# Optimization experiments

Measured on AMD Instinct MI355X. Metric: run time of the kernel, lower is better.

The kernel has to match this reference:

```python
import math
import jax, jax.numpy as jnp
import numpy as np

N_LAYER = 4
D = 192        # n_embd
NH = 4         # n_head
N = 3072       # n_neurons = n_embd * mlp_dim_mult // n_head
VOCAB = 256
BLOCK = 4096
EPS = 1e-5
B, T = 1, 1024


def get_freqs(n, theta=2.0 ** 16):
    t = np.arange(n, dtype=np.float32)
    q = np.floor(t / 2.0) * 2.0  # quantize(t, 2)
    return (1.0 / theta ** (q / n) / (2.0 * math.pi)).astype(np.float32)

_FREQS = jnp.asarray(get_freqs(N))  # [N]


def _ln(x):
    # LayerNorm over last dim, no affine (elementwise_affine=False)
    m = jnp.mean(x, axis=-1, keepdims=True)
    v = jnp.var(x, axis=-1, keepdims=True)
    return (x - m) / jnp.sqrt(v + EPS)


def _rope(x):
    # x: [B, nh, T, N]
    t = x.shape[2]
    phases = (jnp.arange(t, dtype=jnp.float32)[:, None] * _FREQS[None, :]) % 1.0 * (2.0 * math.pi)  # [T, N]
    x_even = x[..., 0::2]
    x_odd = x[..., 1::2]
    v_rot = jnp.stack((-x_odd, x_even), axis=-1).reshape(x.shape)
    return x * jnp.cos(phases) + v_rot * jnp.sin(phases)


def setup_inputs() -> dict:
    key = jax.random.key(0)
    ks = jax.random.split(key, 7)
    s = 0.02
    return {
        "idx": jax.random.randint(ks[0], (B, T), 0, VOCAB, dtype=jnp.int64)
        if jax.config.jax_enable_x64 else jax.random.randint(ks[0], (B, T), 0, VOCAB, dtype=jnp.int32),
        "decoder_x": jax.random.normal(ks[1], (NH, D, N), jnp.float32) * s,
        "decoder_y": jax.random.normal(ks[2], (NH, D, N), jnp.float32) * s,
        "encoder": jax.random.normal(ks[3], (NH * N, D), jnp.float32) * s,
        "embed": jax.random.normal(ks[4], (VOCAB, D), jnp.float32) * s,
        "pos_emb": jax.random.normal(ks[5], (BLOCK, D), jnp.float32) * s,
        "lm_head": jax.random.normal(ks[6], (D, VOCAB), jnp.float32) * s,
    }


def reference(idx, decoder_x, decoder_y, encoder, embed, pos_emb, lm_head):
    b, t = idx.shape
    x = embed[idx] + pos_emb[:t][None]          # [B, T, D]
    x = _ln(x)
    mask = jnp.tril(jnp.ones((t, t), jnp.float32), k=-1)  # strictly lower
    for _ in range(N_LAYER):
        # encoder-side sparsification: D -> N per head
        x_sparse = jax.nn.relu(jnp.einsum('btd,hdn->bhtn', x, decoder_x))  # [B,nh,T,N]
        qr = _rope(x_sparse)
        scores = jnp.einsum('bhtn,bhsn->bhts', qr, qr) * mask              # [B,nh,T,T]
        ykv = _ln(jnp.einsum('bhts,bsd->bhtd', scores, x))                 # [B,nh,T,D]
        y_sparse = jax.nn.relu(jnp.einsum('bhtd,hdn->bhtn', ykv, decoder_y))
        xy = x_sparse * y_sparse                                           # [B,nh,T,N]
        # [B,T,nh*N] @ [nh*N, D]
        ymlp = jnp.einsum('bhtn,hnd->btd', xy, encoder.reshape(NH, N, D))
        x = _ln(x + _ln(ymlp))
    logits = jnp.einsum('btd,dv->btv', x, lm_head)                         # [B,T,vocab]
    return logits
```

## Files before the change

### kernel.cpp

```cpp
#include <hip/hip_runtime.h>
#include <hip/hip_bf16.h>

using bf16 = __hip_bfloat16;

#define D_DIM   192
#define N_DIM   3072
#define NHEAD   4
#define T_SEQ   1024
#define HN      12288
#define NP2     1536
#define VOCABSZ 256
#define NLAYER  4
#define LN_EPS  1e-5f
#define TWO_PI  6.2831853071795864f

typedef __attribute__((ext_vector_type(8)))  short          s16x8;
typedef __attribute__((ext_vector_type(8)))  unsigned short u16x8;
typedef __attribute__((ext_vector_type(4)))  float          f32x4;
typedef __attribute__((ext_vector_type(16))) float          f32x16;

__device__ __forceinline__ float b2f(bf16 v) { return __bfloat162float(v); }
__device__ __forceinline__ float us2f(unsigned short u) {
    unsigned int x = ((unsigned int)u) << 16;
    return __builtin_bit_cast(float, x);
}
__device__ __forceinline__ unsigned short f2us(float f) {
    bf16 b = __float2bfloat16(f);
    return __builtin_bit_cast(unsigned short, b);
}

__global__ void fill_out(float* __restrict__ out, float val, int nelem) {
    int i = blockIdx.x * 256 + threadIdx.x;
    if (i < nelem) out[i] = val;
}

__global__ void t_cvt(const float* __restrict__ in, bf16* __restrict__ out,
                      int R, int C, long inZ, long outZ) {
    __shared__ float tile[64][65];
    in  += inZ  * blockIdx.z;
    out += outZ * blockIdx.z;
    const int tx = threadIdx.x & 63, ty = threadIdx.x >> 6;
    const int r0 = blockIdx.y * 64, c0 = blockIdx.x * 64;
    #pragma unroll
    for (int rr = 0; rr < 16; rr++) {
        int row = ty * 16 + rr;
        tile[row][tx] = in[(size_t)(r0 + row) * C + c0 + tx];
    }
    __syncthreads();
    #pragma unroll
    for (int rr = 0; rr < 16; rr++) {
        int row = ty * 16 + rr;
        out[(size_t)(c0 + row) * R + r0 + tx] = __float2bfloat16(tile[tx][row]);
    }
}

__device__ __forceinline__ void wave_sum2(float& s, float& ss) {
    #pragma unroll
    for (int off = 1; off < 64; off <<= 1) {
        s  += __shfl_xor(s,  off, 64);
        ss += __shfl_xor(ss, off, 64);
    }
}

__global__ void k_embed(const int* __restrict__ idx, const float* __restrict__ emb,
                        const float* __restrict__ pos, float* __restrict__ x,
                        bf16* __restrict__ xb) {
    int t = blockIdx.x, l = threadIdx.x;
    int tok = idx[t];
    const float* e = emb + tok * D_DIM;
    const float* p = pos + t * D_DIM;
    float v0 = e[l] + p[l], v1 = e[l + 64] + p[l + 64], v2 = e[l + 128] + p[l + 128];
    float s = v0 + v1 + v2, ss = v0 * v0 + v1 * v1 + v2 * v2;
    wave_sum2(s, ss);
    float m = s / D_DIM, r = rsqrtf(ss / D_DIM - m * m + LN_EPS);
    float* xr = x + t * D_DIM;
    bf16*  xo = xb + (size_t)t * D_DIM;
    float o0 = (v0 - m) * r, o1 = (v1 - m) * r, o2 = (v2 - m) * r;
    xr[l] = o0; xr[l + 64] = o1; xr[l + 128] = o2;
    xo[l] = __float2bfloat16(o0);
    xo[l + 64] = __float2bfloat16(o1);
    xo[l + 128] = __float2bfloat16(o2);
}

__global__ void k_ln(float* __restrict__ buf) {
    int l = threadIdx.x;
    float* row = buf + (size_t)blockIdx.x * D_DIM;
    float v0 = row[l], v1 = row[l + 64], v2 = row[l + 128];
    float s = v0 + v1 + v2, ss = v0 * v0 + v1 * v1 + v2 * v2;
    wave_sum2(s, ss);
    float m = s / D_DIM, r = rsqrtf(ss / D_DIM - m * m + LN_EPS);
    row[l] = (v0 - m) * r; row[l + 64] = (v1 - m) * r; row[l + 128] = (v2 - m) * r;
}

__global__ void k_ln2b(const float* __restrict__ P0, const float* __restrict__ P1,
                       bf16* __restrict__ outb) {
    int l = threadIdx.x;
    size_t off = (size_t)blockIdx.x * D_DIM;
    const float* r0 = P0 + off;
    const float* r1 = P1 + off;
    float v0 = r0[l] + r1[l];
    float v1 = r0[l + 64] + r1[l + 64];
    float v2 = r0[l + 128] + r1[l + 128];
    float s = v0 + v1 + v2, ss = v0 * v0 + v1 * v1 + v2 * v2;
    wave_sum2(s, ss);
    float m = s / D_DIM, r = rsqrtf(ss / D_DIM - m * m + LN_EPS);
    bf16* o = outb + off;
    o[l]       = __float2bfloat16((v0 - m) * r);
    o[l + 64]  = __float2bfloat16((v1 - m) * r);
    o[l + 128] = __float2bfloat16((v2 - m) * r);
}

template <int NSLAB>
__global__ void k_resid(float* __restrict__ x, const float* __restrict__ P,
                        bf16* __restrict__ xb) {
    int l = threadIdx.x, t = blockIdx.x;
    float y0 = 0.f, y1 = 0.f, y2 = 0.f;
    #pragma unroll
    for (int p = 0; p < NSLAB; p++) {
        const float* r = P + (size_t)p * T_SEQ * D_DIM + (size_t)t * D_DIM;
        y0 += r[l]; y1 += r[l + 64]; y2 += r[l + 128];
    }
    float* xr = x + (size_t)t * D_DIM;
    float s = y0 + y1 + y2, ss = y0 * y0 + y1 * y1 + y2 * y2;
    wave_sum2(s, ss);
    float m1 = s / D_DIM, r1 = rsqrtf(ss / D_DIM - m1 * m1 + LN_EPS);
    float v0 = xr[l] + (y0 - m1) * r1;
    float v1 = xr[l + 64] + (y1 - m1) * r1;
    float v2 = xr[l + 128] + (y2 - m1) * r1;
    s = v0 + v1 + v2; ss = v0 * v0 + v1 * v1 + v2 * v2;
    wave_sum2(s, ss);
    float m2 = s / D_DIM, r2 = rsqrtf(ss / D_DIM - m2 * m2 + LN_EPS);
    float o0 = (v0 - m2) * r2, o1 = (v1 - m2) * r2, o2 = (v2 - m2) * r2;
    xr[l] = o0; xr[l + 64] = o1; xr[l + 128] = o2;
    bf16* xo = xb + (size_t)t * D_DIM;
    xo[l] = __float2bfloat16(o0);
    xo[l + 64] = __float2bfloat16(o1);
    xo[l + 128] = __float2bfloat16(o2);
}

__global__ void k_tables(ushort2* __restrict__ csT) {
    int gid = blockIdx.x * 256 + threadIdx.x;
    int t = gid / NP2, p = gid % NP2;
    float qf = (float)(2 * p);
    float f = exp2f(qf * (-16.0f / 3072.0f)) * (1.0f / (float)TWO_PI);
    float ph = fmodf((float)t * f, 1.0f) * (float)TWO_PI;
    ushort2 cs;
    cs.x = f2us(cosf(ph));
    cs.y = f2us(sinf(ph));
    csT[gid] = cs;
}

__launch_bounds__(256, 4)
__global__ void scores64(const bf16* __restrict__ qr, bf16* __restrict__ sc,
                         bf16* __restrict__ dbuf) {
    const int bid = blockIdx.x;
    const int xcd = bid & 7;
    const int h   = xcd >> 1;
    const int kh  = xcd & 1;
    const int L   = bid >> 3;
    int i = 0;
    while (((i + 1) * (i + 2)) >> 1 <= L) ++i;
    int j = L - ((i * (i + 1)) >> 1);
    const int t0 = i * 64, s0 = j * 64;
    const bool diag = (i == j);

    int arow = t0, brow = s0;
    if (kh == 1 && !diag) { arow = s0; brow = t0; }

    __shared__ short As[2][64][72];
    __shared__ short Bs[2][64][72];

    const int tid = threadIdx.x;
    const int lane = tid & 63, w = tid >> 6;
    const int wtm = (w >> 1) * 32, wtn = (w & 1) * 32;
    const int l31 = lane & 31, lhi = lane >> 5;
    const int r0 = tid >> 2;
    const int kq = (tid & 3) * 16;

    const int kBeg = kh * (N_DIM / 2);
    const bf16* gA = qr + (size_t)(arow + r0) * HN + h * N_DIM + kBeg + kq;
    const bf16* gB = qr + (size_t)(brow + r0) * HN + h * N_DIM + kBeg + kq;

    u16x8 pa0, pa1, pb0, pb1;
    u16x8 qa0, qa1, qb0, qb1;
    auto load0 = [&](int k0) {
        pa0 = *(const u16x8*)(gA + k0);
        pa1 = *(const u16x8*)(gA + k0 + 8);
        pb0 = *(const u16x8*)(gB + k0);
        pb1 = *(const u16x8*)(gB + k0 + 8);
    };
    auto load1 = [&](int k0) {
        qa0 = *(const u16x8*)(gA + k0);
        qa1 = *(const u16x8*)(gA + k0 + 8);
        qb0 = *(const u16x8*)(gB + k0);
        qb1 = *(const u16x8*)(gB + k0 + 8);
    };
    auto dep0 = [&](int buf) {
        *(u16x8*)&As[buf][r0][kq]     = pa0;
        *(u16x8*)&As[buf][r0][kq + 8] = pa1;
        *(u16x8*)&Bs[buf][r0][kq]     = pb0;
        *(u16x8*)&Bs[buf][r0][kq + 8] = pb1;
    };
    auto dep1 = [&](int buf) {
        *(u16x8*)&As[buf][r0][kq]     = qa0;
        *(u16x8*)&As[buf][r0][kq + 8] = qa1;
        *(u16x8*)&Bs[buf][r0][kq]     = qb0;
        *(u16x8*)&Bs[buf][r0][kq + 8] = qb1;
    };

    f32x16 acc;
    #pragma unroll
    for (int r = 0; r < 16; r++) acc[r] = 0.f;

    auto mfma_step = [&](int buf) {
        #pragma unroll
        for (int ks = 0; ks < 4; ks++) {
            s16x8 a = *(const s16x8*)&As[buf][wtm + l31][ks * 16 + lhi * 8];
            s16x8 b = *(const s16x8*)&Bs[buf][wtn + l31][ks * 16 + lhi * 8];
            acc = __builtin_amdgcn_mfma_f32_32x32x16_bf16(a, b, acc, 0, 0, 0);
        }
    };

    const int NIT = (N_DIM / 2) / 64;
    load0(0);
    load1(64);
    dep0(0);
    __syncthreads();

    for (int k = 0; k < NIT; k += 2) {
        if (k + 2 < NIT) load0((k + 2) * 64);
        mfma_step(0);
        if (k + 1 < NIT) dep1(1);
        __syncthreads();
        if (k + 1 < NIT) {
            if (k + 3 < NIT) load1((k + 3) * 64);
            mfma_step(1);
            if (k + 2 < NIT) dep0(0);
            __syncthreads();
        }
    }

    __syncthreads();
    short (*S)[72] = (short(*)[72])&As[0][0][0];
    const bool trS = (kh == 1) && !diag;
    #pragma unroll
    for (int r = 0; r < 16; r++) {
        int rr = wtm + (r & 3) + 8 * (r >> 2) + 4 * lhi;
        int cc = wtn + l31;
        float v = acc[r];
        if (diag && cc >= rr) v = 0.f;
        if (trS) S[cc][rr] = (short)f2us(v);
        else     S[rr][cc] = (short)f2us(v);
    }
    __syncthreads();
    if (kh == 1 && diag) {
        bf16* P = dbuf + (size_t)(h * 16 + i) * 4096;
        #pragma unroll
        for (int e = 0; e < 2; e++) {
            int idxe = tid + e * 256;
            int row = idxe >> 3, cg = (idxe & 7) * 8;
            u16x8 v = *(const u16x8*)&S[row][cg];
            *(u16x8*)(P + row * 64 + cg) = v;
        }
    } else {
        bf16* C = sc + (size_t)h * T_SEQ * T_SEQ;
        #pragma unroll
        for (int e = 0; e < 2; e++) {
            int idxe = tid + e * 256;
            int row = idxe >> 3, cg = (idxe & 7) * 8;
            u16x8 v = *(const u16x8*)&S[row][cg];
            *(u16x8*)(C + (size_t)(arow + row) * T_SEQ + brow + cg) = v;
        }
    }
}

__device__ __forceinline__ void stage_rope8(short* dst, const bf16* src,
                                            const ushort2* csP) {
    u16x8 v  = *(const u16x8*)src;
    u16x8 cs = *(const u16x8*)csP;
    u16x8 o;
    #pragma unroll
    for (int i = 0; i < 4; i++) {
        float e  = us2f(v[2 * i]), od = us2f(v[2 * i + 1]);
        float c  = us2f(cs[2 * i]), s = us2f(cs[2 * i + 1]);
        o[2 * i]     = f2us(e * c - od * s);
        o[2 * i + 1] = f2us(od * c + e * s);
    }
    *(u16x8*)dst = o;
}

__launch_bounds__(256)
__global__ void scores_fused(const bf16* __restrict__ xs,
                             const ushort2* __restrict__ csT,
                             bf16* __restrict__ sc) {
    const int h  = blockIdx.z;
    const int s0 = blockIdx.x * 64, t0 = blockIdx.y * 64;
    if (s0 > t0) return;
    __shared__ short As[64][40];
    __shared__ short Bs[64][40];
    const int tid  = threadIdx.x;
    const int srow = tid >> 2, kq = (tid & 3) * 8;
    const int lane = tid & 63, w = tid >> 6, qd = lane >> 4, lc = lane & 15;
    const int tA = t0 + srow, tB = s0 + srow;
    const bf16* gA = xs + (size_t)tA * HN + h * N_DIM + kq;
    const bf16* gB = xs + (size_t)tB * HN + h * N_DIM + kq;
    const ushort2* cA = csT + (size_t)tA * NP2 + (kq >> 1);
    const ushort2* cB = csT + (size_t)tB * NP2 + (kq >> 1);
    f32x4 acc[4] = {{0.f,0.f,0.f,0.f},{0.f,0.f,0.f,0.f},
                    {0.f,0.f,0.f,0.f},{0.f,0.f,0.f,0.f}};
    for (int k0 = 0; k0 < N_DIM; k0 += 32) {
        stage_rope8(&As[srow][kq], gA + k0, cA + (k0 >> 1));
        stage_rope8(&Bs[srow][kq], gB + k0, cB + (k0 >> 1));
        __syncthreads();
        s16x8 a = *(const s16x8*)&As[w * 16 + lc][qd * 8];
        #pragma unroll
        for (int j = 0; j < 4; j++) {
            s16x8 b = *(const s16x8*)&Bs[j * 16 + lc][qd * 8];
            acc[j] = __builtin_amdgcn_mfma_f32_16x16x32_bf16(a, b, acc[j], 0, 0, 0);
        }
        __syncthreads();
    }
    bf16* C = sc + (size_t)h * T_SEQ * T_SEQ;
    const bool diag = (s0 == t0);
    const int tbase = t0 + w * 16 + qd * 4;
    #pragma unroll
    for (int j = 0; j < 4; j++) {
        int s = s0 + j * 16 + lc;
        #pragma unroll
        for (int r = 0; r < 4; r++) {
            int t = tbase + r;
            C[(size_t)t * T_SEQ + s] =
                __float2bfloat16((!diag || s < t) ? acc[j][r] : 0.f);
        }
    }
}

template <int EPI, bool WQR, typename TA>
__launch_bounds__(256)
__global__ void dgemm128(const TA* __restrict__ A, const bf16* __restrict__ Bt,
                         bf16* __restrict__ xs, bf16* __restrict__ qr,
                         const ushort2* __restrict__ csT) {
    __shared__ __align__(16) short pool[2 * 2 * 128 * 40];
    short (*As)[128][40] = (short(*)[128][40])pool;
    short (*Bs)[128][40] = (short(*)[128][40])(pool + 2 * 128 * 40);

    const int tid = threadIdx.x;
    const int lane = tid & 63, w = tid >> 6;
    const int l31 = lane & 31, lhi = lane >> 5;
    const int wtm = (w >> 1) * 64, wtn = (w & 1) * 64;
    const int n0 = blockIdx.x * 128, m0 = blockIdx.y * 128;
    if constexpr (EPI == 2) A += (size_t)(n0 / N_DIM) * T_SEQ * D_DIM;

    const int r0 = tid >> 2, r1 = r0 + 64;
    const int kq = (tid & 3) * 8;

    const TA*   gA = A  + kq;
    const bf16* gB = Bt + kq;

    float4 fa00, fa01, fa02, fa03, fa10, fa11, fa12, fa13;
    u16x8 ba00, ba01, ba10, ba11;
    u16x8 pb00, pb01, pb10, pb11;
    auto load0 = [&](int k0) {
        if constexpr (__is_same(TA, float)) {
            const TA* a0 = gA + (size_t)(m0 + r0) * D_DIM + k0;
            const TA* a1 = gA + (size_t)(m0 + r1) * D_DIM + k0;
            fa00 = *(const float4*)a0; fa01 = *(const float4*)(a0 + 4);
            fa02 = *(const float4*)a1; fa03 = *(const float4*)(a1 + 4);
        } else {
            ba00 = *(const u16x8*)(gA + (size_t)(m0 + r0) * D_DIM + k0);
            ba01 = *(const u16x8*)(gA + (size_t)(m0 + r1) * D_DIM + k0);
        }
        pb00 = *(const u16x8*)(gB + (size_t)(n0 + r0) * D_DIM + k0);
        pb01 = *(const u16x8*)(gB + (size_t)(n0 + r1) * D_DIM + k0);
    };
    auto load1 = [&](int k0) {
        if constexpr (__is_same(TA, float)) {
            const TA* a0 = gA + (size_t)(m0 + r0) * D_DIM + k0;
            const TA* a1 = gA + (size_t)(m0 + r1) * D_DIM + k0;
            fa10 = *(const float4*)a0; fa11 = *(const float4*)(a0 + 4);
            fa12 = *(const float4*)a1; fa13 = *(const float4*)(a1 + 4);
        } else {
            ba10 = *(const u16x8*)(gA + (size_t)(m0 + r0) * D_DIM + k0);
            ba11 = *(const u16x8*)(gA + (size_t)(m0 + r1) * D_DIM + k0);
        }
        pb10 = *(const u16x8*)(gB + (size_t)(n0 + r0) * D_DIM + k0);
        pb11 = *(const u16x8*)(gB + (size_t)(n0 + r1) * D_DIM + k0);
    };
    auto dep0 = [&](int buf) {
        if constexpr (__is_same(TA, float)) {
            u16x8 o0, o1;
            o0[0] = f2us(fa00.x); o0[1] = f2us(fa00.y); o0[2] = f2us(fa00.z); o0[3] = f2us(fa00.w);
            o0[4] = f2us(fa01.x); o0[5] = f2us(fa01.y); o0[6] = f2us(fa01.z); o0[7] = f2us(fa01.w);
            o1[0] = f2us(fa02.x); o1[1] = f2us(fa02.y); o1[2] = f2us(fa02.z); o1[3] = f2us(fa02.w);
            o1[4] = f2us(fa03.x); o1[5] = f2us(fa03.y); o1[6] = f2us(fa03.z); o1[7] = f2us(fa03.w);
            *(u16x8*)&As[buf][r0][kq] = o0;
            *(u16x8*)&As[buf][r1][kq] = o1;
        } else {
            *(u16x8*)&As[buf][r0][kq] = ba00;
            *(u16x8*)&As[buf][r1][kq] = ba01;
        }
        *(u16x8*)&Bs[buf][r0][kq] = pb00;
        *(u16x8*)&Bs[buf][r1][kq] = pb01;
    };
    auto dep1 = [&](int buf) {
        if constexpr (__is_same(TA, float)) {
            u16x8 o0, o1;
            o0[0] = f2us(fa10.x); o0[1] = f2us(fa10.y); o0[2] = f2us(fa10.z); o0[3] = f2us(fa10.w);
            o0[4] = f2us(fa11.x); o0[5] = f2us(fa11.y); o0[6] = f2us(fa11.z); o0[7] = f2us(fa11.w);
            o1[0] = f2us(fa12.x); o1[1] = f2us(fa12.y); o1[2] = f2us(fa12.z); o1[3] = f2us(fa12.w);
            o1[4] = f2us(fa13.x); o1[5] = f2us(fa13.y); o1[6] = f2us(fa13.z); o1[7] = f2us(fa13.w);
            *(u16x8*)&As[buf][r0][kq] = o0;
            *(u16x8*)&As[buf][r1][kq] = o1;
        } else {
            *(u16x8*)&As[buf][r0][kq] = ba10;
            *(u16x8*)&As[buf][r1][kq] = ba11;
        }
        *(u16x8*)&Bs[buf][r0][kq] = pb10;
        *(u16x8*)&Bs[buf][r1][kq] = pb11;
    };

    f32x16 acc00, acc01, acc10, acc11;
    #pragma unroll
    for (int r = 0; r < 16; r++) { acc00[r] = 0.f; acc01[r] = 0.f; acc10[r] = 0.f; acc11[r] = 0.f; }

    auto mfma_step = [&](int buf) {
        #pragma unroll
        for (int ks = 0; ks < 2; ks++) {
            s16x8 a0 = *(const s16x8*)&As[buf][wtm + l31][ks * 16 + lhi * 8];
            s16x8 a1 = *(const s16x8*)&As[buf][wtm + 32 + l31][ks * 16 + lhi * 8];
            s16x8 b0 = *(const s16x8*)&Bs[buf][wtn + l31][ks * 16 + lhi * 8];
            s16x8 b1 = *(const s16x8*)&Bs[buf][wtn + 32 + l31][ks * 16 + lhi * 8];
            acc00 = __builtin_amdgcn_mfma_f32_32x32x16_bf16(a0, b0, acc00, 0, 0, 0);
            acc01 = __builtin_amdgcn_mfma_f32_32x32x16_bf16(a0, b1, acc01, 0, 0, 0);
            acc10 = __builtin_amdgcn_mfma_f32_32x32x16_bf16(a1, b0, acc10, 0, 0, 0);
            acc11 = __builtin_amdgcn_mfma_f32_32x32x16_bf16(a1, b1, acc11, 0, 0, 0);
        }
    };

    const int NIT = D_DIM / 32;
    load0(0);
    load1(32);
    dep0(0);
    __syncthreads();
    for (int k = 0; k < NIT; k += 2) {
        if (k + 2 < NIT) load0((k + 2) * 32);
        mfma_step(0);
        if (k + 1 < NIT) dep1(1);
        __syncthreads();
        if (k + 1 < NIT) {
            if (k + 3 < NIT) load1((k + 3) * 32);
            mfma_step(1);
            if (k + 2 < NIT) dep0(0);
            __syncthreads();
        }
    }

    short (*S)[136] = (short(*)[136])pool;
    #pragma unroll
    for (int r = 0; r < 16; r++) {
        int rb = (r & 3) + 8 * (r >> 2) + 4 * lhi;
        S[wtm + rb     ][wtn + l31     ] = (short)f2us(fmaxf(acc00[r], 0.f));
        S[wtm + rb     ][wtn + 32 + l31] = (short)f2us(fmaxf(acc01[r], 0.f));
        S[wtm + 32 + rb][wtn + l31     ] = (short)f2us(fmaxf(acc10[r], 0.f));
        S[wtm + 32 + rb][wtn + 32 + l31] = (short)f2us(fmaxf(acc11[r], 0.f));
    }
    __syncthreads();
    #pragma unroll
    for (int e = 0; e < 8; e++) {
        int idxe = tid + e * 256;
        int row = idxe >> 4, cg = idxe & 15;
        u16x8 v = *(const u16x8*)&S[row][cg * 8];
        int t = m0 + row, ngg = n0 + cg * 8;
        size_t ci = (size_t)t * HN + ngg;
        if constexpr (EPI == 1) {
            *(u16x8*)(xs + ci) = v;
            if constexpr (WQR) {
                int p0 = (ngg % N_DIM) >> 1;
                u16x8 cs8 = *(const u16x8*)&csT[(size_t)t * NP2 + p0];
                u16x8 o;
                #pragma unroll
                for (int q = 0; q < 4; q++) {
                    float ev = us2f(v[2 * q]), ov = us2f(v[2 * q + 1]);
                    float c = us2f(cs8[2 * q]), s = us2f(cs8[2 * q + 1]);
                    o[2 * q]     = f2us(ev * c - ov * s);
                    o[2 * q + 1] = f2us(ov * c + ev * s);
                }
                *(u16x8*)(qr + ci) = o;
            }
        } else {
            u16x8 g = *(const u16x8*)(xs + ci);
            u16x8 o;
            #pragma unroll
            for (int q = 0; q < 8; q++) o[q] = f2us(us2f(g[q]) * us2f(v[q]));
            *(u16x8*)(xs + ci) = o;
        }
    }
}

__launch_bounds__(256, 2)
__global__ void gate_ymlp(const bf16* __restrict__ ykvb, const bf16* __restrict__ wY,
                          const bf16* __restrict__ xs, const bf16* __restrict__ wE,
                          float* __restrict__ P) {
    const int bid = blockIdx.x;
    const int s   = (bid & 7) + ((bid >> 7) << 3);
    const int tb  = (bid >> 3) & 15;
    const int t0  = tb * 64;
    const int h   = s >> 2;
    const int ng0 = s * 768;
    const int nh0 = (s & 3) * 768;

    __shared__ __align__(16) short A1s[64][200];
    __shared__ __align__(16) short Bsh[192][72];
    __shared__ __align__(16) short xyA[64][72];
    short (*B1)[200] = (short(*)[200])&Bsh[0][0];

    const int tid = threadIdx.x;
    const int lane = tid & 63, w = tid >> 6;
    const int l31 = lane & 31, lhi = lane >> 5;
    const int wm  = (w >> 1) * 32;
    const int wn1 = (w & 1) * 32;
    const int wn2 = (w & 1) * 96;

    {
        const bf16* src = ykvb + ((size_t)h * T_SEQ + t0 + (tid >> 2)) * D_DIM
                        + (tid & 3) * 48;
        #pragma unroll
        for (int j = 0; j < 6; j++) {
            u16x8 v = *(const u16x8*)(src + j * 8);
            *(u16x8*)&A1s[tid >> 2][(tid & 3) * 48 + j * 8] = v;
        }
    }

    f32x16 oc0, oc1, oc2;
    #pragma unroll
    for (int r = 0; r < 16; r++) { oc0[r] = 0.f; oc1[r] = 0.f; oc2[r] = 0.f; }

    __syncthreads();

    for (int c = 0; c < 12; c++) {
        const int nc = c * 64;
        {
            const bf16* src = wY + ((size_t)h * N_DIM + nh0 + nc + (tid >> 2)) * D_DIM
                            + (tid & 3) * 48;
            #pragma unroll
            for (int j = 0; j < 6; j++) {
                u16x8 v = *(const u16x8*)(src + j * 8);
                *(u16x8*)&B1[tid >> 2][(tid & 3) * 48 + j * 8] = v;
            }
        }
        __syncthreads();
        f32x16 ys;
        #pragma unroll
        for (int r = 0; r < 16; r++) ys[r] = 0.f;
        #pragma unroll
        for (int ks = 0; ks < 12; ks++) {
            s16x8 a = *(const s16x8*)&A1s[wm + l31][ks * 16 + lhi * 8];
            s16x8 b = *(const s16x8*)&B1[wn1 + l31][ks * 16 + lhi * 8];
            ys = __builtin_amdgcn_mfma_f32_32x32x16_bf16(a, b, ys, 0, 0, 0);
        }
        __syncthreads();
        #pragma unroll
        for (int r = 0; r < 16; r++) {
            int rr = wm + (r & 3) + 8 * (r >> 2) + 4 * lhi;
            xyA[rr][wn1 + l31] = (short)f2us(fmaxf(ys[r], 0.f));
        }
        __syncthreads();
        {
            int row = tid >> 2, c0l = (tid & 3) * 16;
            const bf16* sx = xs + (size_t)(t0 + row) * HN + ng0 + nc + c0l;
            #pragma unroll
            for (int e = 0; e < 2; e++) {
                u16x8 g = *(const u16x8*)(sx + e * 8);
                u16x8 y = *(const u16x8*)&xyA[row][c0l + e * 8];
                u16x8 o;
                #pragma unroll
                for (int q = 0; q < 8; q++) o[q] = f2us(us2f(g[q]) * us2f(y[q]));
                *(u16x8*)&xyA[row][c0l + e * 8] = o;
            }
        }
        {
            #pragma unroll
            for (int j = 0; j < 3; j++) {
                int d  = (tid >> 2) * 3 + j;
                int cc = (tid & 3) * 16;
                const bf16* src = wE + (size_t)d * HN + ng0 + nc + cc;
                u16x8 v0 = *(const u16x8*)src;
                u16x8 v1 = *(const u16x8*)(src + 8);
                *(u16x8*)&Bsh[d][cc]     = v0;
                *(u16x8*)&Bsh[d][cc + 8] = v1;
            }
        }
        __syncthreads();
        #pragma unroll
        for (int ks = 0; ks < 4; ks++) {
            s16x8 a  = *(const s16x8*)&xyA[wm + l31][ks * 16 + lhi * 8];
            s16x8 b0 = *(const s16x8*)&Bsh[wn2 + l31     ][ks * 16 + lhi * 8];
            s16x8 b1 = *(const s16x8*)&Bsh[wn2 + 32 + l31][ks * 16 + lhi * 8];
            s16x8 b2 = *(const s16x8*)&Bsh[wn2 + 64 + l31][ks * 16 + lhi * 8];
            oc0 = __builtin_amdgcn_mfma_f32_32x32x16_bf16(a, b0, oc0, 0, 0, 0);
            oc1 = __builtin_amdgcn_mfma_f32_32x32x16_bf16(a, b1, oc1, 0, 0, 0);
            oc2 = __builtin_amdgcn_mfma_f32_32x32x16_bf16(a, b2, oc2, 0, 0, 0);
        }
        __syncthreads();
    }

    float* O = P + (size_t)s * T_SEQ * D_DIM;
    #pragma unroll
    for (int r = 0; r < 16; r++) {
        int rt = t0 + wm + (r & 3) + 8 * (r >> 2) + 4 * lhi;
        O[(size_t)rt * D_DIM + wn2 +      l31] = oc0[r];
        O[(size_t)rt * D_DIM + wn2 + 32 + l31] = oc1[r];
        O[(size_t)rt * D_DIM + wn2 + 64 + l31] = oc2[r];
    }
}

template <typename TA, int MODE>
__launch_bounds__(256)
__global__ void mfma_gemm(const TA* __restrict__ A, const bf16* __restrict__ Bt,
                          float* __restrict__ C, const bf16* __restrict__ aux,
                          int K, int kSeg, int lda, int ldb, int ldc,
                          long aZ, long bZ, long cZ) {
    constexpr bool DUAL = (MODE == 1);
    constexpr int TILES = DUAL ? 6 : 4;
    __shared__ __align__(16) short pool[TILES * 64 * 72];
    short (*As)[64][72] = (short(*)[64][72])pool;
    short (*Bs)[64][72] = (short(*)[64][72])(pool + 2 * 64 * 72);
    short (*Ms)[64][72] = (short(*)[64][72])(pool + 4 * 64 * 72);

    int bx, by, z;
    if constexpr (MODE == 1) {
        const int bid  = blockIdx.x;
        z = bid & 7;
        const int rest = bid >> 3;
        bx = rest % 3;
        by = rest / 3;
    } else {
        bx = blockIdx.x; by = blockIdx.y; z = blockIdx.z;
    }

    const int tid = threadIdx.x;
    const int n0 = bx * 64, m0 = by * 64;
    const int srow = tid >> 2, sk = (tid & 3) * 16;
    const int lane = tid & 63, w = tid >> 6;
    const int l31 = lane & 31, lhi = lane >> 5;
    const int wm = (w >> 1) * 32, wn = (w & 1) * 32;

    int kBeg, kEnd, zh = 0;
    if constexpr (MODE == 1) {
        zh = z >> 1;
        const int seg = z & 1;
        A += aZ * zh;
        C += cZ * zh + bZ * seg;
        const int kc = (m0 + 64 < K) ? m0 + 64 : K;
        const int half0 = ((kc + 127) >> 7) << 6;
        kBeg = seg ? half0 : 0;
        kEnd = seg ? kc : half0;
    } else if constexpr (MODE == 2) {
        A += aZ * z; Bt += bZ * z; C += cZ * z;
        kBeg = z * kSeg; kEnd = kBeg + kSeg;
    } else if constexpr (MODE == 3) {
        A += aZ * z; Bt += bZ * z; C += cZ * z;
        kBeg = 0; kEnd = (m0 + 64 < K) ? m0 + 64 : K;
    } else {
        A += aZ * z; Bt += bZ * z; C += cZ * z;
        kBeg = 0; kEnd = K;
    }

    const TA*   ga = A  + (size_t)(m0 + srow) * lda + sk;
    const bf16* gb = Bt + (size_t)(n0 + srow) * ldb + sk;

    auto msrc = [&](int k0) -> const bf16* {
        if (k0 == m0)
            return aux + (size_t)(zh * 16 + (m0 >> 6)) * 4096
                       + (size_t)srow * 64 + sk;
        return (const bf16*)A + (size_t)(k0 + srow) * lda + m0 + sk;
    };

    float4 f00, f01, f02, f03, f10, f11, f12, f13;
    u16x8 pa00, pa01, pa10, pa11, pb00, pb01, pb10, pb11;
    u16x8 pm00, pm01, pm10, pm11;
    auto load0 = [&](int k0) {
        if constexpr (__is_same(TA, float)) {
            f00 = *(const float4*)(ga + k0);
            f01 = *(const float4*)(ga + k0 + 4);
            f02 = *(const float4*)(ga + k0 + 8);
            f03 = *(const float4*)(ga + k0 + 12);
        } else {
            pa00 = *(const u16x8*)(ga + k0);
            pa01 = *(const u16x8*)(ga + k0 + 8);
        }
        pb00 = *(const u16x8*)(gb + k0);
        pb01 = *(const u16x8*)(gb + k0 + 8);
        if constexpr (DUAL) {
            const bf16* ms = msrc(k0);
            pm00 = *(const u16x8*)ms;
            pm01 = *(const u16x8*)(ms + 8);
        }
    };
    auto load1 = [&](int k0) {
        if constexpr (__is_same(TA, float)) {
            f10 = *(const float4*)(ga + k0);
            f11 = *(const float4*)(ga + k0 + 4);
            f12 = *(const float4*)(ga + k0 + 8);
            f13 = *(const float4*)(ga + k0 + 12);
        } else {
            pa10 = *(const u16x8*)(ga + k0);
            pa11 = *(const u16x8*)(ga + k0 + 8);
        }
        pb10 = *(const u16x8*)(gb + k0);
        pb11 = *(const u16x8*)(gb + k0 + 8);
        if constexpr (DUAL) {
            const bf16* ms = msrc(k0);
            pm10 = *(const u16x8*)ms;
            pm11 = *(const u16x8*)(ms + 8);
        }
    };
    auto dep0 = [&](int buf) {
        if constexpr (__is_same(TA, float)) {
            u16x8 o0, o1;
            o0[0] = f2us(f00.x); o0[1] = f2us(f00.y); o0[2] = f2us(f00.z); o0[3] = f2us(f00.w);
            o0[4] = f2us(f01.x); o0[5] = f2us(f01.y); o0[6] = f2us(f01.z); o0[7] = f2us(f01.w);
            o1[0] = f2us(f02.x); o1[1] = f2us(f02.y); o1[2] = f2us(f02.z); o1[3] = f2us(f02.w);
            o1[4] = f2us(f03.x); o1[5] = f2us(f03.y); o1[6] = f2us(f03.z); o1[7] = f2us(f03.w);
            *(u16x8*)&As[buf][srow][sk]     = o0;
            *(u16x8*)&As[buf][srow][sk + 8] = o1;
        } else {
            *(u16x8*)&As[buf][srow][sk]     = pa00;
            *(u16x8*)&As[buf][srow][sk + 8] = pa01;
        }
        *(u16x8*)&Bs[buf][srow][sk]     = pb00;
        *(u16x8*)&Bs[buf][srow][sk + 8] = pb01;
        if constexpr (DUAL) {
            *(u16x8*)&Ms[buf][srow][sk]     = pm00;
            *(u16x8*)&Ms[buf][srow][sk + 8] = pm01;
        }
    };
    auto dep1 = [&](int buf) {
        if constexpr (__is_same(TA, float)) {
            u16x8 o0, o1;
            o0[0] = f2us(f10.x); o0[1] = f2us(f10.y); o0[2] = f2us(f10.z); o0[3] = f2us(f10.w);
            o0[4] = f2us(f11.x); o0[5] = f2us(f11.y); o0[6] = f2us(f11.z); o0[7] = f2us(f11.w);
            o1[0] = f2us(f12.x); o1[1] = f2us(f12.y); o1[2] = f2us(f12.z); o1[3] = f2us(f12.w);
            o1[4] = f2us(f13.x); o1[5] = f2us(f13.y); o1[6] = f2us(f13.z); o1[7] = f2us(f13.w);
            *(u16x8*)&As[buf][srow][sk]     = o0;
            *(u16x8*)&As[buf][srow][sk + 8] = o1;
        } else {
            *(u16x8*)&As[buf][srow][sk]     = pa10;
            *(u16x8*)&As[buf][srow][sk + 8] = pa11;
        }
        *(u16x8*)&Bs[buf][srow][sk]     = pb10;
        *(u16x8*)&Bs[buf][srow][sk + 8] = pb11;
        if constexpr (DUAL) {
            *(u16x8*)&Ms[buf][srow][sk]     = pm10;
            *(u16x8*)&Ms[buf][srow][sk + 8] = pm11;
        }
    };

    f32x16 acc;
    #pragma unroll
    for (int r = 0; r < 16; r++) acc[r] = 0.f;

    auto mfma_step = [&](int buf) {
        #pragma unroll
        for (int ks = 0; ks < 4; ks++) {
            s16x8 a = *(const s16x8*)&As[buf][wm + l31][ks * 16 + lhi * 8];
            s16x8 b = *(const s16x8*)&Bs[buf][wn + l31][ks * 16 + lhi * 8];
            acc = __builtin_amdgcn_mfma_f32_32x32x16_bf16(a, b, acc, 0, 0, 0);
            if constexpr (DUAL) {
                s16x8 m2 = *(const s16x8*)&Ms[buf][wm + l31][ks * 16 + lhi * 8];
                acc = __builtin_amdgcn_mfma_f32_32x32x16_bf16(m2, b, acc, 0, 0, 0);
            }
        }
    };

    const int NIT = (kEnd - kBeg) >> 6;
    load0(kBeg);
    load1(kBeg + 64);
    dep0(0);
    __syncthreads();

    for (int k = 0; k < NIT; k += 2) {
        if (k + 2 < NIT) load0(kBeg + (k + 2) * 64);
        mfma_step(0);
        if (k + 1 < NIT) dep1(1);
        __syncthreads();
        if (k + 1 < NIT) {
            if (k + 3 < NIT) load1(kBeg + (k + 3) * 64);
            mfma_step(1);
            if (k + 2 < NIT) dep0(0);
            __syncthreads();
        }
    }

    #pragma unroll
    for (int r = 0; r < 16; r++) {
        int row = m0 + wm + (r & 3) + 8 * (r >> 2) + 4 * lhi;
        int col = n0 + wn + l31;
        C[(size_t)row * ldc + col] = acc[r];
    }
}

extern "C" void kernel_launch(void* const* d_in, const int* in_sizes, int n_in,
                              void* d_out, int out_size, void* d_ws, size_t ws_size,
                              hipStream_t stream) {
    const int*   idx   = (const int*)  d_in[0];
    const float* dec_x = (const float*)d_in[1];
    const float* dec_y = (const float*)d_in[2];
    const float* enc   = (const float*)d_in[3];
    const float* emb   = (const float*)d_in[4];
    const float* pose  = (const float*)d_in[5];
    const float* lmh   = (const float*)d_in[6];
    float* out = (float*)d_out;

    char* wp = (char*)d_ws;
    float*   x    = (float*)wp;              wp += (size_t)T_SEQ * D_DIM * 4;
    bf16*    xs   = (bf16*)wp;               wp += (size_t)T_SEQ * HN * 2;
    ushort2* csT  = (ushort2*)wp;            wp += (size_t)T_SEQ * NP2 * 4;
    bf16*    sc   = (bf16*)wp;               wp += (size_t)NHEAD * T_SEQ * T_SEQ * 2;
    float*   ykv  = (float*)wp;              wp += (size_t)NHEAD * T_SEQ * D_DIM * 4;
    float*   ymlp = (float*)wp;              wp += (size_t)T_SEQ * D_DIM * 4;
    bf16*    xT   = (bf16*)wp;               wp += (size_t)D_DIM * T_SEQ * 2;
    bf16*    wX   = (bf16*)wp;               wp += (size_t)NHEAD * N_DIM * D_DIM * 2;
    bf16*    wY   = (bf16*)wp;               wp += (size_t)NHEAD * N_DIM * D_DIM * 2;
    bf16*    wE   = (bf16*)wp;               wp += (size_t)D_DIM * HN * 2;
    bf16*    wL   = (bf16*)wp;               wp += (size_t)VOCABSZ * D_DIM * 2;
    const size_t BASE_NEED = (size_t)(wp - (char*)d_ws);
    bf16*    qr   = (bf16*)wp;
    const size_t FULL_NEED = BASE_NEED + (size_t)T_SEQ * HN * 2;
    bf16*  dbuf  = (bf16*)ymlp;

    if (ws_size < BASE_NEED) {
        fill_out<<<(out_size + 255) / 256, 256, 0, stream>>>(out, (float)ws_size, out_size);
        return;
    }
    const bool USE_QR = (ws_size >= FULL_NEED);

    bf16*  xb_main = (bf16*)sc;
    bf16*  xb_fb   = (bf16*)ymlp;
    float* ymlpP16 = (float*)qr;
    bf16*  ykvb    = (bf16*)((char*)qr + (size_t)16 * T_SEQ * D_DIM * 4);
    float* ymlpP8  = (float*)sc;

    bf16* xb = USE_QR ? xb_main : xb_fb;

    t_cvt<<<dim3(48, 3, 4), 256, 0, stream>>>(dec_x, wX, D_DIM, N_DIM,
                                              (long)D_DIM * N_DIM, (long)N_DIM * D_DIM);
    t_cvt<<<dim3(48, 3, 4), 256, 0, stream>>>(dec_y, wY, D_DIM, N_DIM,
                                              (long)D_DIM * N_DIM, (long)N_DIM * D_DIM);
    t_cvt<<<dim3(3, 192, 1), 256, 0, stream>>>(enc, wE, HN, D_DIM, 0L, 0L);
    t_cvt<<<dim3(4, 3, 1), 256, 0, stream>>>(lmh, wL, D_DIM, VOCABSZ, 0L, 0L);

    k_tables<<<(T_SEQ * NP2) / 256, 256, 0, stream>>>(csT);
    k_embed<<<T_SEQ, 64, 0, stream>>>(idx, emb, pose, x, xb);

    for (int l = 0; l < NLAYER; ++l) {
        t_cvt<<<dim3(3, 16, 1), 256, 0, stream>>>(x, xT, T_SEQ, D_DIM, 0L, 0L);
        if (USE_QR) {
            dgemm128<1, true, bf16><<<dim3(96, 8), 256, 0, stream>>>(xb, wX, xs, qr, csT);
            scores64<<<dim3(1088), 256, 0, stream>>>(qr, sc, dbuf);
            long segZ = (long)((float*)qr - ykv);
            mfma_gemm<bf16, 1><<<dim3(384), 256, 0, stream>>>(
                sc, xT, ykv, dbuf, T_SEQ, 0, T_SEQ, T_SEQ, D_DIM,
                (long)T_SEQ * T_SEQ, segZ, (long)T_SEQ * D_DIM);
            k_ln2b<<<NHEAD * T_SEQ, 64, 0, stream>>>(ykv, (const float*)qr, ykvb);
            gate_ymlp<<<dim3(256), 256, 0, stream>>>(ykvb, wY, xs, wE, ymlpP16);
            k_resid<16><<<T_SEQ, 64, 0, stream>>>(x, ymlpP16, xb);
        } else {
            dgemm128<1, false, bf16><<<dim3(96, 8), 256, 0, stream>>>(xb, wX, xs, qr, csT);
            scores_fused<<<dim3(16, 16, NHEAD), 256, 0, stream>>>(xs, csT, sc);
            mfma_gemm<bf16, 3><<<dim3(3, 16, NHEAD), 256, 0, stream>>>(
                sc, xT, ykv, nullptr, T_SEQ, 0, T_SEQ, T_SEQ, D_DIM,
                (long)T_SEQ * T_SEQ, 0L, (long)T_SEQ * D_DIM);
            k_ln<<<NHEAD * T_SEQ, 64, 0, stream>>>(ykv);
            dgemm128<2, false, float><<<dim3(96, 8), 256, 0, stream>>>(
                ykv, wY, xs, nullptr, nullptr);
            mfma_gemm<bf16, 2><<<dim3(3, 16, 8), 256, 0, stream>>>(
                xs, wE, ymlpP8, nullptr, HN, HN / 8, HN, HN, D_DIM,
                0L, 0L, (long)T_SEQ * D_DIM);
            k_resid<8><<<T_SEQ, 64, 0, stream>>>(x, ymlpP8, xb);
        }
    }

    mfma_gemm<float, 0><<<dim3(4, 16, 1), 256, 0, stream>>>(
        x, wL, out, nullptr, D_DIM, 0, D_DIM, D_DIM, VOCABSZ, 0L, 0L, 0L);
}
```

Measured before the change: 467.9 us.

## Fuse xT transpose into residual LN and fold ykv LayerNorm into gate kernel

Removes the per-layer x transpose kernel by having the embedding and residual LayerNorm kernels write the bf16 transposed copy directly. Also removes the separate k_ln2b kernel by summing the two split-K ykv partials and applying LayerNorm inside gate_ymlp's A-tile load. This cuts kernel launches and an intermediate bf16 buffer round trip. In exchange it adds strided, uncoalesced 2-byte column stores, redundant LN work across blocks sharing the same rows, and more registers in gate_ymlp.

New measurement: 466.4 us. Within noise of the previous version (-0.3%).

```diff
diff --git a/kernel.cpp b/kernel.cpp
--- a/kernel.cpp
+++ b/kernel.cpp
@@ -64,7 +64,7 @@
 
 __global__ void k_embed(const int* __restrict__ idx, const float* __restrict__ emb,
                         const float* __restrict__ pos, float* __restrict__ x,
-                        bf16* __restrict__ xb) {
+                        bf16* __restrict__ xb, bf16* __restrict__ xT) {
     int t = blockIdx.x, l = threadIdx.x;
     int tok = idx[t];
     const float* e = emb + tok * D_DIM;
@@ -77,9 +77,12 @@
     bf16*  xo = xb + (size_t)t * D_DIM;
     float o0 = (v0 - m) * r, o1 = (v1 - m) * r, o2 = (v2 - m) * r;
     xr[l] = o0; xr[l + 64] = o1; xr[l + 128] = o2;
-    xo[l] = __float2bfloat16(o0);
-    xo[l + 64] = __float2bfloat16(o1);
-    xo[l + 128] = __float2bfloat16(o2);
+    bf16 b0 = __float2bfloat16(o0), b1 = __float2bfloat16(o1), b2 = __float2bfloat16(o2);
+    xo[l] = b0; xo[l + 64] = b1; xo[l + 128] = b2;
+    bf16* col = xT + t;
+    col[(size_t)l * T_SEQ]         = b0;
+    col[(size_t)(l + 64) * T_SEQ]  = b1;
+    col[(size_t)(l + 128) * T_SEQ] = b2;
 }
 
 __global__ void k_ln(float* __restrict__ buf) {
@@ -92,27 +95,9 @@
     row[l] = (v0 - m) * r; row[l + 64] = (v1 - m) * r; row[l + 128] = (v2 - m) * r;
 }
 
-__global__ void k_ln2b(const float* __restrict__ P0, const float* __restrict__ P1,
-                       bf16* __restrict__ outb) {
-    int l = threadIdx.x;
-    size_t off = (size_t)blockIdx.x * D_DIM;
-    const float* r0 = P0 + off;
-    const float* r1 = P1 + off;
-    float v0 = r0[l] + r1[l];
-    float v1 = r0[l + 64] + r1[l + 64];
-    float v2 = r0[l + 128] + r1[l + 128];
-    float s = v0 + v1 + v2, ss = v0 * v0 + v1 * v1 + v2 * v2;
-    wave_sum2(s, ss);
-    float m = s / D_DIM, r = rsqrtf(ss / D_DIM - m * m + LN_EPS);
-    bf16* o = outb + off;
-    o[l]       = __float2bfloat16((v0 - m) * r);
-    o[l + 64]  = __float2bfloat16((v1 - m) * r);
-    o[l + 128] = __float2bfloat16((v2 - m) * r);
-}
-
 template <int NSLAB>
 __global__ void k_resid(float* __restrict__ x, const float* __restrict__ P,
-                        bf16* __restrict__ xb) {
+                        bf16* __restrict__ xb, bf16* __restrict__ xT) {
     int l = threadIdx.x, t = blockIdx.x;
     float y0 = 0.f, y1 = 0.f, y2 = 0.f;
     #pragma unroll
@@ -132,10 +117,13 @@
     float m2 = s / D_DIM, r2 = rsqrtf(ss / D_DIM - m2 * m2 + LN_EPS);
     float o0 = (v0 - m2) * r2, o1 = (v1 - m2) * r2, o2 = (v2 - m2) * r2;
     xr[l] = o0; xr[l + 64] = o1; xr[l + 128] = o2;
+    bf16 b0 = __float2bfloat16(o0), b1 = __float2bfloat16(o1), b2 = __float2bfloat16(o2);
     bf16* xo = xb + (size_t)t * D_DIM;
-    xo[l] = __float2bfloat16(o0);
-    xo[l + 64] = __float2bfloat16(o1);
-    xo[l + 128] = __float2bfloat16(o2);
+    xo[l] = b0; xo[l + 64] = b1; xo[l + 128] = b2;
+    bf16* col = xT + t;
+    col[(size_t)l * T_SEQ]         = b0;
+    col[(size_t)(l + 64) * T_SEQ]  = b1;
+    col[(size_t)(l + 128) * T_SEQ] = b2;
 }
 
 __global__ void k_tables(ushort2* __restrict__ csT) {
@@ -498,7 +486,8 @@
 }
 
 __launch_bounds__(256, 2)
-__global__ void gate_ymlp(const bf16* __restrict__ ykvb, const bf16* __restrict__ wY,
+__global__ void gate_ymlp(const float* __restrict__ ykv0, const float* __restrict__ ykv1,
+                          const bf16* __restrict__ wY,
                           const bf16* __restrict__ xs, const bf16* __restrict__ wE,
                           float* __restrict__ P) {
     const int bid = blockIdx.x;
@@ -522,12 +511,30 @@
     const int wn2 = (w & 1) * 96;
 
     {
-        const bf16* src = ykvb + ((size_t)h * T_SEQ + t0 + (tid >> 2)) * D_DIM
-                        + (tid & 3) * 48;
-        #pragma unroll
-        for (int j = 0; j < 6; j++) {
-            u16x8 v = *(const u16x8*)(src + j * 8);
-            *(u16x8*)&A1s[tid >> 2][(tid & 3) * 48 + j * 8] = v;
+        const int row = tid >> 2, q = tid & 3;
+        size_t off = ((size_t)h * T_SEQ + t0 + row) * D_DIM + q * 48;
+        const float* p0 = ykv0 + off;
+        const float* p1 = ykv1 + off;
+        float v[48];
+        float sm = 0.f, ssq = 0.f;
+        #pragma unroll
+        for (int e = 0; e < 12; e++) {
+            float4 a = *(const float4*)(p0 + e * 4);
+            float4 b = *(const float4*)(p1 + e * 4);
+            float c0 = a.x + b.x, c1 = a.y + b.y, c2 = a.z + b.z, c3 = a.w + b.w;
+            v[e * 4 + 0] = c0; v[e * 4 + 1] = c1; v[e * 4 + 2] = c2; v[e * 4 + 3] = c3;
+            sm  += c0 + c1 + c2 + c3;
+            ssq += c0 * c0 + c1 * c1 + c2 * c2 + c3 * c3;
+        }
+        sm  += __shfl_xor(sm, 1, 64);  ssq += __shfl_xor(ssq, 1, 64);
+        sm  += __shfl_xor(sm, 2, 64);  ssq += __shfl_xor(ssq, 2, 64);
+        float m = sm / D_DIM, r = rsqrtf(ssq / D_DIM - m * m + LN_EPS);
+        #pragma unroll
+        for (int e = 0; e < 6; e++) {
+            u16x8 o;
+            #pragma unroll
+            for (int k2 = 0; k2 < 8; k2++) o[k2] = f2us((v[e * 8 + k2] - m) * r);
+            *(u16x8*)&A1s[row][q * 48 + e * 8] = o;
         }
     }
 
@@ -838,7 +845,7 @@
     bf16*  xb_main = (bf16*)sc;
     bf16*  xb_fb   = (bf16*)ymlp;
     float* ymlpP16 = (float*)qr;
-    bf16*  ykvb    = (bf16*)((char*)qr + (size_t)16 * T_SEQ * D_DIM * 4);
+    float* ykvP1   = (float*)((char*)qr + (size_t)16 * T_SEQ * D_DIM * 4);
     float* ymlpP8  = (float*)sc;
 
     bf16* xb = USE_QR ? xb_main : xb_fb;
@@ -851,20 +858,18 @@
     t_cvt<<<dim3(4, 3, 1), 256, 0, stream>>>(lmh, wL, D_DIM, VOCABSZ, 0L, 0L);
 
     k_tables<<<(T_SEQ * NP2) / 256, 256, 0, stream>>>(csT);
-    k_embed<<<T_SEQ, 64, 0, stream>>>(idx, emb, pose, x, xb);
+    k_embed<<<T_SEQ, 64, 0, stream>>>(idx, emb, pose, x, xb, xT);
 
     for (int l = 0; l < NLAYER; ++l) {
-        t_cvt<<<dim3(3, 16, 1), 256, 0, stream>>>(x, xT, T_SEQ, D_DIM, 0L, 0L);
         if (USE_QR) {
             dgemm128<1, true, bf16><<<dim3(96, 8), 256, 0, stream>>>(xb, wX, xs, qr, csT);
             scores64<<<dim3(1088), 256, 0, stream>>>(qr, sc, dbuf);
-            long segZ = (long)((float*)qr - ykv);
+            long segZ = (long)(ykvP1 - ykv);
             mfma_gemm<bf16, 1><<<dim3(384), 256, 0, stream>>>(
                 sc, xT, ykv, dbuf, T_SEQ, 0, T_SEQ, T_SEQ, D_DIM,
                 (long)T_SEQ * T_SEQ, segZ, (long)T_SEQ * D_DIM);
-            k_ln2b<<<NHEAD * T_SEQ, 64, 0, stream>>>(ykv, (const float*)qr, ykvb);
-            gate_ymlp<<<dim3(256), 256, 0, stream>>>(ykvb, wY, xs, wE, ymlpP16);
-            k_resid<16><<<T_SEQ, 64, 0, stream>>>(x, ymlpP16, xb);
+            gate_ymlp<<<dim3(256), 256, 0, stream>>>(ykv, ykvP1, wY, xs, wE, ymlpP16);
+            k_resid<16><<<T_SEQ, 64, 0, stream>>>(x, ymlpP16, xb, xT);
         } else {
             dgemm128<1, false, bf16><<<dim3(96, 8), 256, 0, stream>>>(xb, wX, xs, qr, csT);
             scores_fused<<<dim3(16, 16, NHEAD), 256, 0, stream>>>(xs, csT, sc);
@@ -877,7 +882,7 @@
             mfma_gemm<bf16, 2><<<dim3(3, 16, 8), 256, 0, stream>>>(
                 xs, wE, ymlpP8, nullptr, HN, HN / 8, HN, HN, D_DIM,
                 0L, 0L, (long)T_SEQ * D_DIM);
-            k_resid<8><<<T_SEQ, 64, 0, stream>>>(x, ymlpP8, xb);
+            k_resid<8><<<T_SEQ, 64, 0, stream>>>(x, ymlpP8, xb, xT);
         }
     }
 
```
